# Kernel optimization log

Measured on AMD Instinct MI355X. Metric: run time of the kernel, lower is better.

## Reference

```python
import jax, jax.numpy as jnp
import numpy as np

B, S, H, NH, PF, L = 2, 2048, 1024, 16, 4096, 6
HD = H // NH
EPS = 1e-5


def setup_inputs() -> dict:
    key = jax.random.key(0)
    ks = jax.random.split(key, 12)
    s = lambda k, shp, fan: jax.random.normal(k, shp, jnp.float32) * (1.0 / np.sqrt(fan))
    return {
        "input_tensor": jax.random.normal(ks[0], (B, S, H), jnp.float32),
        "pos_emb": s(ks[1], (S, H), H),
        "Wq": s(ks[2], (L, H, H), H), "bq": jnp.zeros((L, H), jnp.float32),
        "Wk": s(ks[3], (L, H, H), H), "bk": jnp.zeros((L, H), jnp.float32),
        "Wv": s(ks[4], (L, H, H), H), "bv": jnp.zeros((L, H), jnp.float32),
        "Wo": s(ks[5], (L, H, H), H), "bo": jnp.zeros((L, H), jnp.float32),
        "ln_g": jnp.ones((L, H), jnp.float32), "ln_b": jnp.zeros((L, H), jnp.float32),
        "W1": s(ks[6], (L, H, PF), H), "b1": jnp.zeros((L, PF), jnp.float32),
        "W2": s(ks[7], (L, PF, H), PF), "b2": jnp.zeros((L, H), jnp.float32),
    }


def _layernorm(x, g, b):
    mu = jnp.mean(x, axis=-1, keepdims=True)
    var = jnp.mean(jnp.square(x - mu), axis=-1, keepdims=True)
    return (x - mu) * jax.lax.rsqrt(var + EPS) * g + b


def _encoder(input_tensor, pos_emb, params):
    # pos embed: same positions for every batch row
    src = input_tensor * jnp.sqrt(jnp.float32(H)) + pos_emb[None, :, :]

    def layer(src, p):
        Wq, bq, Wk, bk, Wv, bv, Wo, bo, g, b, W1, b1, W2, b2 = p
        q = (src @ Wq + bq).reshape(B, S, NH, HD)
        k = (src @ Wk + bk).reshape(B, S, NH, HD)
        v = (src @ Wv + bv).reshape(B, S, NH, HD)
        # scores [B, NH, S, S]
        energy = jnp.einsum("bqhd,bkhd->bhqk", q, k) / jnp.sqrt(jnp.float32(HD))
        attn = jax.nn.softmax(energy, axis=-1)
        ctx = jnp.einsum("bhqk,bkhd->bqhd", attn, v).reshape(B, S, H)
        attn_out = ctx @ Wo + bo
        src = _layernorm(src + attn_out, g, b)
        ffn = jax.nn.relu(src @ W1 + b1) @ W2 + b2
        src = _layernorm(src + ffn, g, b)  # same LayerNorm reused, as in source
        return src, None

    src, _ = jax.lax.scan(layer, src, params)
    return src


def reference(input_tensor, pos_emb, Wq, bq, Wk, bk, Wv, bv, Wo, bo, ln_g, ln_b, W1, b1, W2, b2):
    params = (Wq, bq, Wk, bk, Wv, bv, Wo, bo, ln_g, ln_b, W1, b1, W2, b2)
    return _encoder(input_tensor, pos_emb, params)
```

## Files before the change

kernel.cpp:

```cpp
#include <hip/hip_runtime.h>
#include <cstdint>

constexpr int Bc = 2, Sc = 2048, Hc = 1024, NHc = 16, HDc = 64, PFc = 4096, Lc = 6;
constexpr float EPSc = 1e-5f;
constexpr float QSC = 0.18033688011112042f;

using f32x4  = __attribute__((ext_vector_type(4))) float;
using bf16x8 = __attribute__((ext_vector_type(8))) __bf16;
using bf16x4 = __attribute__((ext_vector_type(4))) __bf16;
using u32x4  = __attribute__((ext_vector_type(4))) unsigned;

#if __has_builtin(__builtin_amdgcn_exp2f)
#define EXP2(x) __builtin_amdgcn_exp2f(x)
#else
#define EXP2(x) exp2f(x)
#endif

__device__ __forceinline__ f32x4 mfma16(bf16x8 a, bf16x8 b, f32x4 c) {
    return __builtin_amdgcn_mfma_f32_16x16x32_bf16(a, b, c, 0, 0, 0);
}

__device__ __forceinline__ void gload_lds16(const void* g, void* l) {
    __builtin_amdgcn_global_load_lds(
        (__attribute__((address_space(1))) void*)(uintptr_t)g,
        (__attribute__((address_space(3))) void*)(uint32_t)(uintptr_t)l,
        16, 0, 0);
}

struct HL { __bf16 h, l; };
__device__ __forceinline__ HL split2(float v) {
    HL r;
    r.h = (__bf16)v;
    r.l = (__bf16)(v - (float)r.h);
    return r;
}

__device__ __forceinline__ unsigned bfbits(__bf16 x) {
    return (unsigned)__builtin_bit_cast(unsigned short, x);
}
__device__ __forceinline__ unsigned packbf(float a, float b) {
    return bfbits((__bf16)a) | (bfbits((__bf16)b) << 16);
}

__global__ __launch_bounds__(256) void wconv_kernel(
    const float* __restrict__ in, __bf16* __restrict__ out, int K, int N)
{
    __shared__ float tile[64][65];
    const int t = threadIdx.x;
    const size_t lstride = (size_t)K * N;
    const float* ip = in + (size_t)blockIdx.z * lstride;
    __bf16* op = out + (size_t)blockIdx.z * lstride;
    const int n0 = blockIdx.x * 64, k0 = blockIdx.y * 64;
    #pragma unroll
    for (int c = 0; c < 4; ++c) {
        int idx = c * 256 + t;
        int row = idx >> 4;
        int c4  = idx & 15;
        float4 v = *(const float4*)(ip + (size_t)(k0 + row) * N + n0 + c4 * 4);
        tile[row][c4 * 4 + 0] = v.x; tile[row][c4 * 4 + 1] = v.y;
        tile[row][c4 * 4 + 2] = v.z; tile[row][c4 * 4 + 3] = v.w;
    }
    __syncthreads();
    #pragma unroll
    for (int c = 0; c < 4; ++c) {
        int idx = c * 256 + t;
        int n  = idx >> 4;
        int k4 = idx & 15;
        bf16x4 hh = { (__bf16)tile[k4 * 4 + 0][n], (__bf16)tile[k4 * 4 + 1][n],
                      (__bf16)tile[k4 * 4 + 2][n], (__bf16)tile[k4 * 4 + 3][n] };
        *(bf16x4*)(op + (size_t)(n0 + n) * K + k0 + k4 * 4) = hh;
    }
}

__global__ __launch_bounds__(256) void embed_kernel(
    const float* __restrict__ in, const float* __restrict__ pos,
    float* __restrict__ sf, __bf16* __restrict__ sh, __bf16* __restrict__ sl)
{
    const int n4 = (Bc * Sc * Hc) / 4;
    const int pmask = (Sc * Hc / 4) - 1;
    for (int i = blockIdx.x * 256 + threadIdx.x; i < n4; i += gridDim.x * 256) {
        float4 a = ((const float4*)in)[i];
        float4 p = ((const float4*)pos)[i & pmask];
        float4 r;
        r.x = a.x * 32.f + p.x; r.y = a.y * 32.f + p.y;
        r.z = a.z * 32.f + p.z; r.w = a.w * 32.f + p.w;
        ((float4*)sf)[i] = r;
        HL e0 = split2(r.x), e1 = split2(r.y), e2 = split2(r.z), e3 = split2(r.w);
        bf16x4 hh = { e0.h, e1.h, e2.h, e3.h };
        bf16x4 ll = { e0.l, e1.l, e2.l, e3.l };
        ((bf16x4*)sh)[i] = hh;
        ((bf16x4*)sl)[i] = ll;
    }
}

template<int BM, int OUTMODE, bool RELU>
__global__ __launch_bounds__(256) void gemm_bt_kernel(
    const __bf16* __restrict__ A, const __bf16* __restrict__ Wt,
    const float* __restrict__ bias, void* __restrict__ out,
    int M, int N, int K)
{
    constexpr int MI = BM / 32;
    __shared__ alignas(16) __bf16 Alds[2][BM * 64];
    __shared__ alignas(16) __bf16 Blds[2][128 * 64];

    const int tid = threadIdx.x, lane = tid & 63, wave = tid >> 6;
    const int lr = lane & 15, lg = lane >> 4;
    const int m0 = blockIdx.y * BM, n0 = blockIdx.x * 128;
    const int wm = (wave >> 1) * (BM / 2), wn = (wave & 1) * 64;

    f32x4 acc[MI][4] = {};

    auto stage = [&](int k0, int buf) {
        #pragma unroll
        for (int c = 0; c < BM / 32; ++c) {
            int li = c * 256 + tid;
            int row = li >> 3;
            int lcb = ((li & 7) << 4) ^ ((row & 7) << 4);
            gload_lds16(A + (size_t)(m0 + row) * K + k0 + (lcb >> 1),
                        (char*)Alds[buf] + (size_t)(c * 256 + wave * 64) * 16);
        }
        #pragma unroll
        for (int c = 0; c < 4; ++c) {
            int li = c * 256 + tid;
            int row = li >> 3;
            int lcb = ((li & 7) << 4) ^ ((row & 7) << 4);
            gload_lds16(Wt + (size_t)(n0 + row) * K + k0 + (lcb >> 1),
                        (char*)Blds[buf] + (size_t)(c * 256 + wave * 64) * 16);
        }
    };

    stage(0, 0);
    __syncthreads();
    int cur = 0;

    for (int k0 = 0; k0 < K; k0 += 64) {
        if (k0 + 64 < K) stage(k0 + 64, cur ^ 1);

        bf16x8 af[2][MI], bfr[2][4];
        #pragma unroll
        for (int ks = 0; ks < 2; ++ks) {
            #pragma unroll
            for (int i = 0; i < MI; ++i) {
                int ra = wm + i * 16 + lr;
                int pa = (ks * 64 + lg * 16) ^ ((ra & 7) << 4);
                af[ks][i] = *(const bf16x8*)((const char*)Alds[cur] + ra * 128 + pa);
            }
            #pragma unroll
            for (int i = 0; i < 4; ++i) {
                int rb = wn + i * 16 + lr;
                int pb = (ks * 64 + lg * 16) ^ ((rb & 7) << 4);
                bfr[ks][i] = *(const bf16x8*)((const char*)Blds[cur] + rb * 128 + pb);
            }
        }
        #pragma unroll
        for (int ks = 0; ks < 2; ++ks)
            #pragma unroll
            for (int mi = 0; mi < MI; ++mi)
                #pragma unroll
                for (int ni = 0; ni < 4; ++ni)
                    acc[mi][ni] = mfma16(af[ks][mi], bfr[ks][ni], acc[mi][ni]);

        __syncthreads();
        cur ^= 1;
    }

    #pragma unroll
    for (int ni = 0; ni < 4; ++ni) {
        int col = n0 + wn + ni * 16 + lr;
        float bv = bias[col];
        #pragma unroll
        for (int mi = 0; mi < MI; ++mi) {
            int rowb = m0 + wm + mi * 16 + lg * 4;
            #pragma unroll
            for (int r = 0; r < 4; ++r) {
                float v = acc[mi][ni][r] + bv;
                if (RELU) v = fmaxf(v, 0.f);
                size_t idx = (size_t)(rowb + r) * N + col;
                if constexpr (OUTMODE == 0) ((float*)out)[idx] = v;
                else                        ((__bf16*)out)[idx] = (__bf16)v;
            }
        }
    }
}

struct QKVBT {
    const __bf16 *wq, *wk, *wv;
    const float *bq, *bk, *bv;
    __bf16 *q, *k, *v;
};

__global__ __launch_bounds__(256) void qkv_bt_kernel(
    const __bf16* __restrict__ A, QKVBT a)
{
    constexpr int N = Hc, K = Hc;
    __shared__ alignas(16) __bf16 Alds[2][128 * 64];
    __shared__ alignas(16) __bf16 Blds[2][128 * 64];

    const int tid = threadIdx.x, lane = tid & 63, wave = tid >> 6;
    const int lr = lane & 15, lg = lane >> 4;
    const int gx = blockIdx.x;
    const int widx = gx >> 3;
    const int n0 = (gx & 7) * 128;
    const int m0 = blockIdx.y * 128;
    const int wm = (wave >> 1) * 64, wn = (wave & 1) * 64;

    const __bf16* Wt  = (widx == 0) ? a.wq : (widx == 1) ? a.wk : a.wv;
    const float* bias = (widx == 0) ? a.bq : (widx == 1) ? a.bk : a.bv;

    f32x4 acc[4][4] = {};

    auto stage = [&](int k0, int buf) {
        #pragma unroll
        for (int c = 0; c < 4; ++c) {
            int li = c * 256 + tid;
            int row = li >> 3;
            int lcb = ((li & 7) << 4) ^ ((row & 7) << 4);
            gload_lds16(A + (size_t)(m0 + row) * K + k0 + (lcb >> 1),
                        (char*)Alds[buf] + (size_t)(c * 256 + wave * 64) * 16);
            gload_lds16(Wt + (size_t)(n0 + row) * K + k0 + (lcb >> 1),
                        (char*)Blds[buf] + (size_t)(c * 256 + wave * 64) * 16);
        }
    };

    stage(0, 0);
    __syncthreads();
    int cur = 0;

    for (int k0 = 0; k0 < K; k0 += 64) {
        if (k0 + 64 < K) stage(k0 + 64, cur ^ 1);

        bf16x8 af[2][4], bfr[2][4];
        #pragma unroll
        for (int ks = 0; ks < 2; ++ks) {
            #pragma unroll
            for (int i = 0; i < 4; ++i) {
                int ra = wm + i * 16 + lr;
                int pa = (ks * 64 + lg * 16) ^ ((ra & 7) << 4);
                af[ks][i] = *(const bf16x8*)((const char*)Alds[cur] + ra * 128 + pa);
                int rb = wn + i * 16 + lr;
                int pb = (ks * 64 + lg * 16) ^ ((rb & 7) << 4);
                bfr[ks][i] = *(const bf16x8*)((const char*)Blds[cur] + rb * 128 + pb);
            }
        }
        #pragma unroll
        for (int ks = 0; ks < 2; ++ks)
            #pragma unroll
            for (int mi = 0; mi < 4; ++mi)
                #pragma unroll
                for (int ni = 0; ni < 4; ++ni)
                    acc[mi][ni] = mfma16(af[ks][mi], bfr[ks][ni], acc[mi][ni]);

        __syncthreads();
        cur ^= 1;
    }

    __bf16* outp = (widx == 0) ? a.q : (widx == 1) ? a.k : a.v;
    const float osc = (widx == 0) ? QSC : 1.f;
    #pragma unroll
    for (int ni = 0; ni < 4; ++ni) {
        int col = n0 + wn + ni * 16 + lr;
        float bv = bias[col];
        int hh = col >> 6, d = col & 63;
        #pragma unroll
        for (int mi = 0; mi < 4; ++mi) {
            int rowb = m0 + wm + mi * 16 + lg * 4;
            #pragma unroll
            for (int r = 0; r < 4; ++r) {
                int row = rowb + r;
                int bb = row >> 11, s = row & (Sc - 1);
                outp[((size_t)(bb * NHc + hh) * Sc + s) * HDc + d] =
                    (__bf16)((acc[mi][ni][r] + bv) * osc);
            }
        }
    }
}

struct QKVArgs {
    const float *Wq, *Wk, *Wv, *bq, *bk, *bv;
    __bf16 *qh, *ql, *kh, *kl, *vv;
};

__global__ __launch_bounds__(256) void qkv0_kernel(
    const __bf16* __restrict__ Ahi, const __bf16* __restrict__ Alo, QKVArgs a)
{
    constexpr int N = Hc, K = Hc;
    __shared__ alignas(16) __bf16 AldsH[128 * 64];
    __shared__ alignas(16) __bf16 AldsL[128 * 64];
    __shared__ alignas(16) __bf16 BldsH[128 * 64];
    __shared__ alignas(16) __bf16 BldsL[128 * 64];

    const int tid  = threadIdx.x;
    const int lane = tid & 63;
    const int wave = tid >> 6;
    const int lr   = lane & 15;
    const int lg   = lane >> 4;
    const int gx   = blockIdx.x;
    const int widx = gx >> 3;
    const int n0   = (gx & 7) * 128;
    const int m0   = blockIdx.y * 128;
    const int wm   = (wave >> 1) * 64;
    const int wn   = (wave & 1) * 64;
    const int bn   = tid & 127;
    const int bkh  = (tid >> 7) * 32;

    const float* Bw   = (widx == 0) ? a.Wq : (widx == 1) ? a.Wk : a.Wv;
    const float* bias = (widx == 0) ? a.bq : (widx == 1) ? a.bk : a.bv;

    f32x4 acc[4][4] = {};
    const float* bsrc0 = Bw + (size_t)bkh * N + n0 + bn;

    for (int k0 = 0; k0 < K; k0 += 64) {
        #pragma unroll
        for (int c = 0; c < 4; ++c) {
            int li  = c * 256 + tid;
            int row = li >> 3;
            int lcb = ((li & 7) << 4) ^ ((row & 7) << 4);
            size_t goff = (size_t)(m0 + row) * K + k0 + (lcb >> 1);
            size_t loff = (size_t)(c * 256 + wave * 64) * 16;
            gload_lds16(Ahi + goff, (char*)AldsH + loff);
            gload_lds16(Alo + goff, (char*)AldsL + loff);
        }
        const float* bs = bsrc0 + (size_t)k0 * N;
        #pragma unroll
        for (int c = 0; c < 4; ++c) {
            bf16x8 ph, plv;
            #pragma unroll
            for (int j = 0; j < 8; ++j) {
                HL e = split2(bs[(size_t)(c * 8 + j) * N]);
                ph[j] = e.h;
                plv[j] = e.l;
            }
            int pcb = (bkh * 2 + c * 16) ^ ((bn & 7) << 4);
            *(bf16x8*)((char*)BldsH + bn * 128 + pcb) = ph;
            *(bf16x8*)((char*)BldsL + bn * 128 + pcb) = plv;
        }
        __syncthreads();

        bf16x8 ah[2][4], al[2][4], bh[2][4], bl[2][4];
        #pragma unroll
        for (int ks = 0; ks < 2; ++ks) {
            #pragma unroll
            for (int i = 0; i < 4; ++i) {
                int ra = wm + i * 16 + lr;
                int pa = (ks * 64 + lg * 16) ^ ((ra & 7) << 4);
                ah[ks][i] = *(const bf16x8*)((const char*)AldsH + ra * 128 + pa);
                al[ks][i] = *(const bf16x8*)((const char*)AldsL + ra * 128 + pa);
                int rb = wn + i * 16 + lr;
                int pb = (ks * 64 + lg * 16) ^ ((rb & 7) << 4);
                bh[ks][i] = *(const bf16x8*)((const char*)BldsH + rb * 128 + pb);
                bl[ks][i] = *(const bf16x8*)((const char*)BldsL + rb * 128 + pb);
            }
        }
        #pragma unroll
        for (int ks = 0; ks < 2; ++ks)
            #pragma unroll
            for (int mi = 0; mi < 4; ++mi)
                #pragma unroll
                for (int ni = 0; ni < 4; ++ni) {
                    acc[mi][ni] = mfma16(ah[ks][mi], bh[ks][ni], acc[mi][ni]);
                    acc[mi][ni] = mfma16(al[ks][mi], bh[ks][ni], acc[mi][ni]);
                    acc[mi][ni] = mfma16(ah[ks][mi], bl[ks][ni], acc[mi][ni]);
                }
        __syncthreads();
    }

    __bf16* outh = (widx == 0) ? a.qh : (widx == 1) ? a.kh : a.vv;
    __bf16* outl = (widx == 0) ? a.ql : a.kl;
    const float osc = (widx == 0) ? QSC : 1.f;
    #pragma unroll
    for (int ni = 0; ni < 4; ++ni) {
        int col = n0 + wn + ni * 16 + lr;
        float bv = bias[col];
        int hh = col >> 6, d = col & 63;
        #pragma unroll
        for (int mi = 0; mi < 4; ++mi) {
            int rowb = m0 + wm + mi * 16 + lg * 4;
            #pragma unroll
            for (int r = 0; r < 4; ++r) {
                int row = rowb + r;
                int bb = row >> 11, s = row & (Sc - 1);
                size_t idx = ((size_t)(bb * NHc + hh) * Sc + s) * HDc + d;
                float v = (acc[mi][ni][r] + bv) * osc;
                if (widx < 2) {
                    HL e = split2(v);
                    outh[idx] = e.h;
                    outl[idx] = e.l;
                } else {
                    outh[idx] = (__bf16)v;
                }
            }
        }
    }
}

template<int QKSPLIT>
__global__ __launch_bounds__(256) void attn_kernel(
    const __bf16* __restrict__ Qh, const __bf16* __restrict__ Ql,
    const __bf16* __restrict__ Kh, const __bf16* __restrict__ Kl,
    const __bf16* __restrict__ V, __bf16* __restrict__ O)
{
    __shared__ alignas(16) __bf16 Ksh[2][64 * 64];
    __shared__ alignas(16) __bf16 Klo[QKSPLIT ? 2 : 1][QKSPLIT ? 64 * 64 : 8];
    __shared__ alignas(16) __bf16 VT[2][64 * 64];

    const int tid = threadIdx.x;
    const int lane = tid & 63, wave = tid >> 6;
    const int lr = lane & 15, lg = lane >> 4;
    const int h = blockIdx.y, b = blockIdx.z;
    const int q0 = blockIdx.x * 128 + wave * 32;

    const size_t headoff = ((size_t)b * NHc + h) * Sc * HDc;
    const __bf16* Qb  = Qh + headoff;
    const __bf16* Kb  = Kh + headoff;
    const __bf16* Klb = QKSPLIT ? (Kl + headoff) : nullptr;
    const __bf16* Vb  = V + headoff;

    const size_t qrowA = (size_t)(q0 + lr) * HDc;
    const size_t qrowB = qrowA + 16 * HDc;
    bf16x8 qfA0 = *(const bf16x8*)(Qb + qrowA + lg * 8);
    bf16x8 qfA1 = *(const bf16x8*)(Qb + qrowA + 32 + lg * 8);
    bf16x8 qfB0 = *(const bf16x8*)(Qb + qrowB + lg * 8);
    bf16x8 qfB1 = *(const bf16x8*)(Qb + qrowB + 32 + lg * 8);
    bf16x8 qlA0, qlA1, qlB0, qlB1;
    if constexpr (QKSPLIT) {
        const __bf16* Qlb = Ql + headoff;
        qlA0 = *(const bf16x8*)(Qlb + qrowA + lg * 8);
        qlA1 = *(const bf16x8*)(Qlb + qrowA + 32 + lg * 8);
        qlB0 = *(const bf16x8*)(Qlb + qrowB + lg * 8);
        qlB1 = *(const bf16x8*)(Qlb + qrowB + 32 + lg * 8);
    }

    const int kp = tid & 31, dblk = tid >> 5;
    const int sp = (kp & 0x11) | ((kp & 0x06) << 1) | ((kp & 0x08) >> 2);

    auto stageK = [&](int kt, int buf) {
        #pragma unroll
        for (int c = 0; c < 2; ++c) {
            int li  = c * 256 + tid;
            int row = li >> 3;
            int lcb = ((li & 7) << 4) ^ ((row & 7) << 4);
            size_t goff = (size_t)(kt * 64 + row) * HDc + (lcb >> 1);
            size_t loff = (size_t)(c * 256 + wave * 64) * 16;
            gload_lds16(Kb + goff, (char*)Ksh[buf] + loff);
            if constexpr (QKSPLIT)
                gload_lds16(Klb + goff, (char*)Klo[buf] + loff);
        }
    };
    auto loadV = [&](int kt, bf16x8& va, bf16x8& vb2) {
        const __bf16* vs = Vb + (size_t)(kt * 64 + 2 * kp) * HDc + dblk * 8;
        va  = *(const bf16x8*)vs;
        vb2 = *(const bf16x8*)(vs + HDc);
    };
    auto writeVT = [&](int buf, bf16x8 va, bf16x8 vb2) {
        #pragma unroll
        for (int j = 0; j < 8; ++j) {
            int d = dblk * 8 + j;
            unsigned u = bfbits(va[j]) | (bfbits(vb2[j]) << 16);
            int byte = d * 128 + ((sp * 4) ^ ((d & 7) << 4));
            *(unsigned*)((char*)VT[buf] + byte) = u;
        }
    };

    f32x4 oA[4] = {}, oB[4] = {};
    float mA = -1e30f, mB = -1e30f, lsA = 0.f, lsB = 0.f;

    stageK(0, 0);
    {
        bf16x8 va, vb2;
        loadV(0, va, vb2);
        writeVT(0, va, vb2);
    }
    __syncthreads();

    int cur = 0;
    for (int kt = 0; kt < Sc / 64; ++kt) {
        const int nb = cur ^ 1;
        const bool pf = (kt + 1 < Sc / 64);
        bf16x8 va, vb2;
        if (pf) {
            stageK(kt + 1, nb);
            loadV(kt + 1, va, vb2);
        }

        const char* Kc = (const char*)Ksh[cur];
        const char* Klc = (const char*)Klo[QKSPLIT ? cur : 0];
        f32x4 sA[4], sB[4];
        #pragma unroll
        for (int kg = 0; kg < 4; ++kg) {
            int ra = kg * 16 + lr;
            int pa0 = (lg * 16) ^ ((ra & 7) << 4);
            int pa1 = (64 + lg * 16) ^ ((ra & 7) << 4);
            bf16x8 kf0 = *(const bf16x8*)(Kc + ra * 128 + pa0);
            bf16x8 kf1 = *(const bf16x8*)(Kc + ra * 128 + pa1);
            f32x4 tA = {}, tB = {};
            tA = mfma16(kf0, qfA0, tA);
            tA = mfma16(kf1, qfA1, tA);
            tB = mfma16(kf0, qfB0, tB);
            tB = mfma16(kf1, qfB1, tB);
            if constexpr (QKSPLIT) {
                bf16x8 kg0 = *(const bf16x8*)(Klc + ra * 128 + pa0);
                bf16x8 kg1 = *(const bf16x8*)(Klc + ra * 128 + pa1);
                tA = mfma16(kg0, qfA0, tA);
                tA = mfma16(kg1, qfA1, tA);
                tA = mfma16(kf0, qlA0, tA);
                tA = mfma16(kf1, qlA1, tA);
                tB = mfma16(kg0, qfB0, tB);
                tB = mfma16(kg1, qfB1, tB);
                tB = mfma16(kf0, qlB0, tB);
                tB = mfma16(kf1, qlB1, tB);
            }
            sA[kg] = tA;
            sB[kg] = tB;
        }

        float mtA = -1e30f, mtB = -1e30f;
        #pragma unroll
        for (int kg = 0; kg < 4; ++kg)
            #pragma unroll
            for (int r = 0; r < 4; ++r) {
                mtA = fmaxf(mtA, sA[kg][r]);
                mtB = fmaxf(mtB, sB[kg][r]);
            }
        mtA = fmaxf(mtA, __shfl_xor(mtA, 16));
        mtA = fmaxf(mtA, __shfl_xor(mtA, 32));
        mtB = fmaxf(mtB, __shfl_xor(mtB, 16));
        mtB = fmaxf(mtB, __shfl_xor(mtB, 32));
        if (!__all(mtA <= mA)) {
            float mnew = fmaxf(mA, mtA);
            float fac = EXP2(mA - mnew);
            mA = mnew;
            lsA *= fac;
            #pragma unroll
            for (int r = 0; r < 4; ++r) {
                float fr = __shfl(fac, (lg << 4) | (lg * 4 + r));
                #pragma unroll
                for (int nd = 0; nd < 4; ++nd) oA[nd][r] *= fr;
            }
        }
        if (!__all(mtB <= mB)) {
            float mnew = fmaxf(mB, mtB);
            float fac = EXP2(mB - mnew);
            mB = mnew;
            lsB *= fac;
            #pragma unroll
            for (int r = 0; r < 4; ++r) {
                float fr = __shfl(fac, (lg << 4) | (lg * 4 + r));
                #pragma unroll
                for (int nd = 0; nd < 4; ++nd) oB[nd][r] *= fr;
            }
        }
        float psA = 0.f, psB = 0.f;
        #pragma unroll
        for (int kg = 0; kg < 4; ++kg)
            #pragma unroll
            for (int r = 0; r < 4; ++r) {
                float pA = EXP2(sA[kg][r] - mA);
                float pB = EXP2(sB[kg][r] - mB);
                psA += pA;
                psB += pB;
                sA[kg][r] = pA;
                sB[kg][r] = pB;
            }
        psA += __shfl_xor(psA, 16);
        psA += __shfl_xor(psA, 32);
        psB += __shfl_xor(psB, 16);
        psB += __shfl_xor(psB, 32);
        lsA += psA;
        lsB += psB;

        #pragma unroll
        for (int kh2 = 0; kh2 < 2; ++kh2) {
            u32x4 pkA, pkB;
            pkA[0] = packbf(sA[2 * kh2][0],     sA[2 * kh2][1]);
            pkA[1] = packbf(sA[2 * kh2][2],     sA[2 * kh2][3]);
            pkA[2] = packbf(sA[2 * kh2 + 1][0], sA[2 * kh2 + 1][1]);
            pkA[3] = packbf(sA[2 * kh2 + 1][2], sA[2 * kh2 + 1][3]);
            pkB[0] = packbf(sB[2 * kh2][0],     sB[2 * kh2][1]);
            pkB[1] = packbf(sB[2 * kh2][2],     sB[2 * kh2][3]);
            pkB[2] = packbf(sB[2 * kh2 + 1][0], sB[2 * kh2 + 1][1]);
            pkB[3] = packbf(sB[2 * kh2 + 1][2], sB[2 * kh2 + 1][3]);
            bf16x8 pafA = __builtin_bit_cast(bf16x8, pkA);
            bf16x8 pafB = __builtin_bit_cast(bf16x8, pkB);
            #pragma unroll
            for (int nd = 0; nd < 4; ++nd) {
                int d = nd * 16 + lr;
                int byte = d * 128 + ((64 * kh2 + 16 * lg) ^ ((d & 7) << 4));
                bf16x8 vbf = *(const bf16x8*)((const char*)VT[cur] + byte);
                oA[nd] = mfma16(pafA, vbf, oA[nd]);
                oB[nd] = mfma16(pafB, vbf, oB[nd]);
            }
        }

        if (pf) writeVT(nb, va, vb2);
        __syncthreads();
        cur = nb;
    }

    #pragma unroll
    for (int r = 0; r < 4; ++r) {
        float lvA = __shfl(lsA, (lg << 4) | (lg * 4 + r));
        float lvB = __shfl(lsB, (lg << 4) | (lg * 4 + r));
        float invA = 1.f / lvA;
        float invB = 1.f / lvB;
        size_t orowA = ((size_t)b * Sc + q0 + lg * 4 + r) * Hc + h * HDc;
        size_t orowB = orowA + (size_t)16 * Hc;
        #pragma unroll
        for (int nd = 0; nd < 4; ++nd) {
            O[orowA + nd * 16 + lr] = (__bf16)(oA[nd][r] * invA);
            O[orowB + nd * 16 + lr] = (__bf16)(oB[nd][r] * invB);
        }
    }
}

__global__ __launch_bounds__(256) void ln_kernel(
    const float* __restrict__ xr, const __bf16* __restrict__ y,
    const float* __restrict__ g, const float* __restrict__ beta,
    float* __restrict__ of, __bf16* __restrict__ oh)
{
    __shared__ float red[2][4];
    const int row = blockIdx.x, t = threadIdx.x;
    const int lane = t & 63, wave = t >> 6;
    const int idx = row * 256 + t;
    float4 a = ((const float4*)xr)[idx];
    bf16x4 cb = ((const bf16x4*)y)[idx];
    float4 v;
    v.x = a.x + (float)cb[0]; v.y = a.y + (float)cb[1];
    v.z = a.z + (float)cb[2]; v.w = a.w + (float)cb[3];
    float s1 = v.x + v.y + v.z + v.w;
    float s2 = v.x * v.x + v.y * v.y + v.z * v.z + v.w * v.w;
    #pragma unroll
    for (int off = 1; off < 64; off <<= 1) {
        s1 += __shfl_xor(s1, off);
        s2 += __shfl_xor(s2, off);
    }
    if (lane == 0) { red[0][wave] = s1; red[1][wave] = s2; }
    __syncthreads();
    s1 = red[0][0] + red[0][1] + red[0][2] + red[0][3];
    s2 = red[1][0] + red[1][1] + red[1][2] + red[1][3];
    const float mu   = s1 * (1.f / Hc);
    const float var  = s2 * (1.f / Hc) - mu * mu;
    const float rstd = rsqrtf(var + EPSc);
    float4 gg = ((const float4*)g)[t];
    float4 bb = ((const float4*)beta)[t];
    float4 r;
    r.x = (v.x - mu) * rstd * gg.x + bb.x;
    r.y = (v.y - mu) * rstd * gg.y + bb.y;
    r.z = (v.z - mu) * rstd * gg.z + bb.z;
    r.w = (v.w - mu) * rstd * gg.w + bb.w;
    ((float4*)of)[idx] = r;
    bf16x4 hh = { (__bf16)r.x, (__bf16)r.y, (__bf16)r.z, (__bf16)r.w };
    ((bf16x4*)oh)[idx] = hh;
}

extern "C" void kernel_launch(void* const* d_in, const int* in_sizes, int n_in,
                              void* d_out, int out_size, void* d_ws, size_t ws_size,
                              hipStream_t stream)
{
    const float* inp = (const float*)d_in[0];
    const float* pos = (const float*)d_in[1];
    const float* Wq  = (const float*)d_in[2];
    const float* bq  = (const float*)d_in[3];
    const float* Wk  = (const float*)d_in[4];
    const float* bk  = (const float*)d_in[5];
    const float* Wv  = (const float*)d_in[6];
    const float* bv  = (const float*)d_in[7];
    const float* Wo  = (const float*)d_in[8];
    const float* bo  = (const float*)d_in[9];
    const float* lng = (const float*)d_in[10];
    const float* lnb = (const float*)d_in[11];
    const float* W1  = (const float*)d_in[12];
    const float* b1  = (const float*)d_in[13];
    const float* W2  = (const float*)d_in[14];
    const float* b2  = (const float*)d_in[15];

    char* ws = (char*)d_ws;
    const size_t MB = 1u << 20;
    float*  src_f = (float*)(ws);
    __bf16* src_h = (__bf16*)(ws + 16 * MB);
    __bf16* src_l = (__bf16*)(ws + 24 * MB);
    __bf16* qh    = (__bf16*)(ws + 32 * MB);
    __bf16* kh    = (__bf16*)(ws + 40 * MB);
    __bf16* vv    = (__bf16*)(ws + 48 * MB);
    __bf16* ctx   = (__bf16*)(ws + 56 * MB);
    __bf16* ql    = (__bf16*)(ws + 64 * MB);
    __bf16* kl    = (__bf16*)(ws + 72 * MB);
    __bf16* tmpb  = (__bf16*)(ws + 80 * MB);
    __bf16* h1    = (__bf16*)(ws + 32 * MB);
    __bf16* wqT   = (__bf16*)(ws + 96 * MB);
    __bf16* wkT   = (__bf16*)(ws + 108 * MB);
    __bf16* wvT   = (__bf16*)(ws + 120 * MB);
    __bf16* woT   = (__bf16*)(ws + 132 * MB);
    __bf16* w1T   = (__bf16*)(ws + 144 * MB);
    __bf16* w2T   = (__bf16*)(ws + 192 * MB);

    const int M = Bc * Sc;

    wconv_kernel<<<dim3(16, 16, 6), 256, 0, stream>>>(Wq, wqT, Hc, Hc);
    wconv_kernel<<<dim3(16, 16, 6), 256, 0, stream>>>(Wk, wkT, Hc, Hc);
    wconv_kernel<<<dim3(16, 16, 6), 256, 0, stream>>>(Wv, wvT, Hc, Hc);
    wconv_kernel<<<dim3(16, 16, 6), 256, 0, stream>>>(Wo, woT, Hc, Hc);
    wconv_kernel<<<dim3(64, 16, 6), 256, 0, stream>>>(W1, w1T, Hc, PFc);
    wconv_kernel<<<dim3(16, 64, 6), 256, 0, stream>>>(W2, w2T, PFc, Hc);

    embed_kernel<<<2048, 256, 0, stream>>>(inp, pos, src_f, src_h, src_l);

    for (int l = 0; l < Lc; ++l) {
        const size_t wHH = (size_t)l * Hc * Hc;
        const size_t wH  = (size_t)l * Hc;
        if (l == 0) {
            QKVArgs qa = { Wq, Wk, Wv, bq, bk, bv, qh, ql, kh, kl, vv };
            qkv0_kernel<<<dim3(24, 32), 256, 0, stream>>>(src_h, src_l, qa);
            attn_kernel<1><<<dim3(16, 16, 2), 256, 0, stream>>>(qh, ql, kh, kl, vv, ctx);
        } else {
            QKVBT qa = { wqT + wHH, wkT + wHH, wvT + wHH, bq + wH, bk + wH, bv + wH,
                         qh, kh, vv };
            qkv_bt_kernel<<<dim3(24, 32), 256, 0, stream>>>(src_h, qa);
            attn_kernel<0><<<dim3(16, 16, 2), 256, 0, stream>>>(qh, nullptr, kh, nullptr, vv, ctx);
        }
        gemm_bt_kernel<64, 1, false><<<dim3(8, 64), 256, 0, stream>>>(
            ctx, woT + wHH, bo + wH, tmpb, M, Hc, Hc);
        ln_kernel<<<M, 256, 0, stream>>>(src_f, tmpb, lng + wH, lnb + wH, src_f, src_h);
        gemm_bt_kernel<128, 1, true><<<dim3(32, 32), 256, 0, stream>>>(
            src_h, w1T + (size_t)l * Hc * PFc, b1 + (size_t)l * PFc, h1, M, PFc, Hc);
        gemm_bt_kernel<64, 1, false><<<dim3(8, 64), 256, 0, stream>>>(
            h1, w2T + (size_t)l * PFc * Hc, b2 + wH, tmpb, M, Hc, PFc);
        float* dst = (l == Lc - 1) ? (float*)d_out : src_f;
        ln_kernel<<<M, 256, 0, stream>>>(src_f, tmpb, lng + wH, lnb + wH, dst, src_h);
    }
}
```

Baseline: 1.697 ms.

## Pre-split layer-0 Q/K weights, skip split for V, add XCD block swizzle

Measured after the change: 1.608 ms. 1.06x faster.

```diff
diff --git a/kernel.cpp b/kernel.cpp
--- a/kernel.cpp
+++ b/kernel.cpp
@@ -40,6 +40,10 @@
 }
 __device__ __forceinline__ unsigned packbf(float a, float b) {
     return bfbits((__bf16)a) | (bfbits((__bf16)b) << 16);
+}
+
+__device__ __forceinline__ int xcd_swz(int bid, int nwg) {
+    return (bid & 7) * (nwg >> 3) + (bid >> 3);
 }
 
 __global__ __launch_bounds__(256) void wconv_kernel(
@@ -69,6 +73,39 @@
         bf16x4 hh = { (__bf16)tile[k4 * 4 + 0][n], (__bf16)tile[k4 * 4 + 1][n],
                       (__bf16)tile[k4 * 4 + 2][n], (__bf16)tile[k4 * 4 + 3][n] };
         *(bf16x4*)(op + (size_t)(n0 + n) * K + k0 + k4 * 4) = hh;
+    }
+}
+
+__global__ __launch_bounds__(256) void wconv2_kernel(
+    const float* __restrict__ in, __bf16* __restrict__ outh,
+    __bf16* __restrict__ outl, int K, int N)
+{
+    __shared__ float tile[64][65];
+    const int t = threadIdx.x;
+    const int n0 = blockIdx.x * 64, k0 = blockIdx.y * 64;
+    #pragma unroll
+    for (int c = 0; c < 4; ++c) {
+        int idx = c * 256 + t;
+        int row = idx >> 4;
+        int c4  = idx & 15;
+        float4 v = *(const float4*)(in + (size_t)(k0 + row) * N + n0 + c4 * 4);
+        tile[row][c4 * 4 + 0] = v.x; tile[row][c4 * 4 + 1] = v.y;
+        tile[row][c4 * 4 + 2] = v.z; tile[row][c4 * 4 + 3] = v.w;
+    }
+    __syncthreads();
+    #pragma unroll
+    for (int c = 0; c < 4; ++c) {
+        int idx = c * 256 + t;
+        int n  = idx >> 4;
+        int k4 = idx & 15;
+        HL e0 = split2(tile[k4 * 4 + 0][n]);
+        HL e1 = split2(tile[k4 * 4 + 1][n]);
+        HL e2 = split2(tile[k4 * 4 + 2][n]);
+        HL e3 = split2(tile[k4 * 4 + 3][n]);
+        bf16x4 hh = { e0.h, e1.h, e2.h, e3.h };
+        bf16x4 ll = { e0.l, e1.l, e2.l, e3.l };
+        *(bf16x4*)(outh + (size_t)(n0 + n) * K + k0 + k4 * 4) = hh;
+        *(bf16x4*)(outl + (size_t)(n0 + n) * K + k0 + k4 * 4) = ll;
     }
 }
 
@@ -105,7 +142,9 @@
 
     const int tid = threadIdx.x, lane = tid & 63, wave = tid >> 6;
     const int lr = lane & 15, lg = lane >> 4;
-    const int m0 = blockIdx.y * BM, n0 = blockIdx.x * 128;
+    const int nbx = gridDim.x;
+    const int swz = xcd_swz(blockIdx.y * nbx + blockIdx.x, nbx * gridDim.y);
+    const int m0 = (swz / nbx) * BM, n0 = (swz % nbx) * 128;
     const int wm = (wave >> 1) * (BM / 2), wn = (wave & 1) * 64;
 
     f32x4 acc[MI][4] = {};
@@ -198,10 +237,12 @@
 
     const int tid = threadIdx.x, lane = tid & 63, wave = tid >> 6;
     const int lr = lane & 15, lg = lane >> 4;
-    const int gx = blockIdx.x;
+    const int nbx = gridDim.x;
+    const int swz = xcd_swz(blockIdx.y * nbx + blockIdx.x, nbx * gridDim.y);
+    const int gx = swz % nbx;
     const int widx = gx >> 3;
     const int n0 = (gx & 7) * 128;
-    const int m0 = blockIdx.y * 128;
+    const int m0 = (swz / nbx) * 128;
     const int wm = (wave >> 1) * 64, wn = (wave & 1) * 64;
 
     const __bf16* Wt  = (widx == 0) ? a.wq : (widx == 1) ? a.wk : a.wv;
@@ -275,13 +316,14 @@
     }
 }
 
-struct QKVArgs {
-    const float *Wq, *Wk, *Wv, *bq, *bk, *bv;
+struct QKV0S {
+    const __bf16 *wqh, *wql, *wkh, *wkl, *wv;
+    const float *bq, *bk, *bv;
     __bf16 *qh, *ql, *kh, *kl, *vv;
 };
 
-__global__ __launch_bounds__(256) void qkv0_kernel(
-    const __bf16* __restrict__ Ahi, const __bf16* __restrict__ Alo, QKVArgs a)
+__global__ __launch_bounds__(256) void qkv0s_kernel(
+    const __bf16* __restrict__ Ahi, const __bf16* __restrict__ Alo, QKV0S a)
 {
     constexpr int N = Hc, K = Hc;
     __shared__ alignas(16) __bf16 AldsH[128 * 64];
@@ -289,50 +331,38 @@
     __shared__ alignas(16) __bf16 BldsH[128 * 64];
     __shared__ alignas(16) __bf16 BldsL[128 * 64];
 
-    const int tid  = threadIdx.x;
-    const int lane = tid & 63;
-    const int wave = tid >> 6;
-    const int lr   = lane & 15;
-    const int lg   = lane >> 4;
-    const int gx   = blockIdx.x;
+    const int tid = threadIdx.x, lane = tid & 63, wave = tid >> 6;
+    const int lr = lane & 15, lg = lane >> 4;
+    const int nbx = gridDim.x;
+    const int swz = xcd_swz(blockIdx.y * nbx + blockIdx.x, nbx * gridDim.y);
+    const int gx = swz % nbx;
     const int widx = gx >> 3;
-    const int n0   = (gx & 7) * 128;
-    const int m0   = blockIdx.y * 128;
-    const int wm   = (wave >> 1) * 64;
-    const int wn   = (wave & 1) * 64;
-    const int bn   = tid & 127;
-    const int bkh  = (tid >> 7) * 32;
-
-    const float* Bw   = (widx == 0) ? a.Wq : (widx == 1) ? a.Wk : a.Wv;
+    const int n0 = (gx & 7) * 128;
+    const int m0 = (swz / nbx) * 128;
+    const int wm = (wave >> 1) * 64, wn = (wave & 1) * 64;
+    const bool SPLIT = (widx < 2);
+
+    const __bf16* Bh = (widx == 0) ? a.wqh : (widx == 1) ? a.wkh : a.wv;
+    const __bf16* Bl = (widx == 0) ? a.wql : a.wkl;
     const float* bias = (widx == 0) ? a.bq : (widx == 1) ? a.bk : a.bv;
 
     f32x4 acc[4][4] = {};
-    const float* bsrc0 = Bw + (size_t)bkh * N + n0 + bn;
 
     for (int k0 = 0; k0 < K; k0 += 64) {
         #pragma unroll
         for (int c = 0; c < 4; ++c) {
-            int li  = c * 256 + tid;
+            int li = c * 256 + tid;
             int row = li >> 3;
             int lcb = ((li & 7) << 4) ^ ((row & 7) << 4);
-            size_t goff = (size_t)(m0 + row) * K + k0 + (lcb >> 1);
+            size_t aoff = (size_t)(m0 + row) * K + k0 + (lcb >> 1);
+            size_t boff = (size_t)(n0 + row) * K + k0 + (lcb >> 1);
             size_t loff = (size_t)(c * 256 + wave * 64) * 16;
-            gload_lds16(Ahi + goff, (char*)AldsH + loff);
-            gload_lds16(Alo + goff, (char*)AldsL + loff);
-        }
-        const float* bs = bsrc0 + (size_t)k0 * N;
-        #pragma unroll
-        for (int c = 0; c < 4; ++c) {
-            bf16x8 ph, plv;
-            #pragma unroll
-            for (int j = 0; j < 8; ++j) {
-                HL e = split2(bs[(size_t)(c * 8 + j) * N]);
-                ph[j] = e.h;
-                plv[j] = e.l;
-            }
-            int pcb = (bkh * 2 + c * 16) ^ ((bn & 7) << 4);
-            *(bf16x8*)((char*)BldsH + bn * 128 + pcb) = ph;
-            *(bf16x8*)((char*)BldsL + bn * 128 + pcb) = plv;
+            gload_lds16(Ahi + aoff, (char*)AldsH + loff);
+            gload_lds16(Bh + boff, (char*)BldsH + loff);
+            if (SPLIT) {
+                gload_lds16(Alo + aoff, (char*)AldsL + loff);
+                gload_lds16(Bl + boff, (char*)BldsL + loff);
+            }
         }
         __syncthreads();
 
@@ -344,11 +374,13 @@
                 int ra = wm + i * 16 + lr;
                 int pa = (ks * 64 + lg * 16) ^ ((ra & 7) << 4);
                 ah[ks][i] = *(const bf16x8*)((const char*)AldsH + ra * 128 + pa);
-                al[ks][i] = *(const bf16x8*)((const char*)AldsL + ra * 128 + pa);
                 int rb = wn + i * 16 + lr;
                 int pb = (ks * 64 + lg * 16) ^ ((rb & 7) << 4);
                 bh[ks][i] = *(const bf16x8*)((const char*)BldsH + rb * 128 + pb);
-                bl[ks][i] = *(const bf16x8*)((const char*)BldsL + rb * 128 + pb);
+                if (SPLIT) {
+                    al[ks][i] = *(const bf16x8*)((const char*)AldsL + ra * 128 + pa);
+                    bl[ks][i] = *(const bf16x8*)((const char*)BldsL + rb * 128 + pb);
+                }
             }
         }
         #pragma unroll
@@ -358,8 +390,10 @@
                 #pragma unroll
                 for (int ni = 0; ni < 4; ++ni) {
                     acc[mi][ni] = mfma16(ah[ks][mi], bh[ks][ni], acc[mi][ni]);
-                    acc[mi][ni] = mfma16(al[ks][mi], bh[ks][ni], acc[mi][ni]);
-                    acc[mi][ni] = mfma16(ah[ks][mi], bl[ks][ni], acc[mi][ni]);
+                    if (SPLIT) {
+                        acc[mi][ni] = mfma16(al[ks][mi], bh[ks][ni], acc[mi][ni]);
+                        acc[mi][ni] = mfma16(ah[ks][mi], bl[ks][ni], acc[mi][ni]);
+                    }
                 }
         __syncthreads();
     }
@@ -381,7 +415,7 @@
                 int bb = row >> 11, s = row & (Sc - 1);
                 size_t idx = ((size_t)(bb * NHc + hh) * Sc + s) * HDc + d;
                 float v = (acc[mi][ni][r] + bv) * osc;
-                if (widx < 2) {
+                if (SPLIT) {
                     HL e = split2(v);
                     outh[idx] = e.h;
                     outl[idx] = e.l;
@@ -685,6 +719,10 @@
     __bf16* ql    = (__bf16*)(ws + 64 * MB);
     __bf16* kl    = (__bf16*)(ws + 72 * MB);
     __bf16* tmpb  = (__bf16*)(ws + 80 * MB);
+    __bf16* wq0h  = (__bf16*)(ws + 80 * MB);
+    __bf16* wq0l  = (__bf16*)(ws + 82 * MB);
+    __bf16* wk0h  = (__bf16*)(ws + 84 * MB);
+    __bf16* wk0l  = (__bf16*)(ws + 86 * MB);
     __bf16* h1    = (__bf16*)(ws + 32 * MB);
     __bf16* wqT   = (__bf16*)(ws + 96 * MB);
     __bf16* wkT   = (__bf16*)(ws + 108 * MB);
@@ -701,6 +739,8 @@
     wconv_kernel<<<dim3(16, 16, 6), 256, 0, stream>>>(Wo, woT, Hc, Hc);
     wconv_kernel<<<dim3(64, 16, 6), 256, 0, stream>>>(W1, w1T, Hc, PFc);
     wconv_kernel<<<dim3(16, 64, 6), 256, 0, stream>>>(W2, w2T, PFc, Hc);
+    wconv2_kernel<<<dim3(16, 16), 256, 0, stream>>>(Wq, wq0h, wq0l, Hc, Hc);
+    wconv2_kernel<<<dim3(16, 16), 256, 0, stream>>>(Wk, wk0h, wk0l, Hc, Hc);
 
     embed_kernel<<<2048, 256, 0, stream>>>(inp, pos, src_f, src_h, src_l);
 
@@ -708,8 +748,9 @@
         const size_t wHH = (size_t)l * Hc * Hc;
         const size_t wH  = (size_t)l * Hc;
         if (l == 0) {
-            QKVArgs qa = { Wq, Wk, Wv, bq, bk, bv, qh, ql, kh, kl, vv };
-            qkv0_kernel<<<dim3(24, 32), 256, 0, stream>>>(src_h, src_l, qa);
+            QKV0S qa = { wq0h, wq0l, wk0h, wk0l, wvT, bq, bk, bv,
+                         qh, ql, kh, kl, vv };
+            qkv0s_kernel<<<dim3(24, 32), 256, 0, stream>>>(src_h, src_l, qa);
             attn_kernel<1><<<dim3(16, 16, 2), 256, 0, stream>>>(qh, ql, kh, kl, vv, ctx);
         } else {
             QKVBT qa = { wqT + wHH, wkT + wHH, wvT + wHH, bq + wH, bk + wH, bv + wH,
```
